# Optimization experiments

Measured on AMD Instinct MI355X. Metric: run time of the kernel, lower is better.

Reference implementation:

```python
import jax, jax.numpy as jnp
import numpy as np

ALPHA, GAMMA, EPS = 0.25, 2.0, 1e-8


def _safe_div(num, den):
    # tf.math.divide_no_nan semantics
    return jnp.where(den > 0, num / jnp.where(den > 0, den, 1.0), 0.0)


def giou_loss(b1, b2):
    """tfa.losses.giou_loss: boxes [ymin, xmin, ymax, xmax], broadcastable
    leading dims; returns 1 - GIoU."""
    b1_ymin, b1_xmin, b1_ymax, b1_xmax = jnp.split(b1, 4, axis=-1)
    b2_ymin, b2_xmin, b2_ymax, b2_xmax = jnp.split(b2, 4, axis=-1)
    b1_area = jnp.maximum(b1_ymax - b1_ymin, 0.0) * jnp.maximum(b1_xmax - b1_xmin, 0.0)
    b2_area = jnp.maximum(b2_ymax - b2_ymin, 0.0) * jnp.maximum(b2_xmax - b2_xmin, 0.0)
    i_ymin = jnp.maximum(b1_ymin, b2_ymin)
    i_xmin = jnp.maximum(b1_xmin, b2_xmin)
    i_ymax = jnp.minimum(b1_ymax, b2_ymax)
    i_xmax = jnp.minimum(b1_xmax, b2_xmax)
    inter = jnp.maximum(i_ymax - i_ymin, 0.0) * jnp.maximum(i_xmax - i_xmin, 0.0)
    union = b1_area + b2_area - inter
    iou = _safe_div(inter, union)
    e_ymin = jnp.minimum(b1_ymin, b2_ymin)
    e_xmin = jnp.minimum(b1_xmin, b2_xmin)
    e_ymax = jnp.maximum(b1_ymax, b2_ymax)
    e_xmax = jnp.maximum(b1_xmax, b2_xmax)
    enclose = jnp.maximum(e_ymax - e_ymin, 0.0) * jnp.maximum(e_xmax - e_xmin, 0.0)
    giou = iou - _safe_div(enclose - union, enclose)
    return (1.0 - giou)[..., 0]  # squeeze the split-kept last dim


def setup_inputs() -> dict:
    key = jax.random.key(0)
    k1, k2, k3, k4 = jax.random.split(key, 4)
    b, n, C, m = 8, 16384, 80, 100
    return {
        "cls_pred": jax.random.uniform(k1, (b, n, C), dtype=jnp.float32),
        "loc_pred": jax.random.uniform(k2, (b, n, 4), dtype=jnp.float32),
        "cls_true": jax.random.randint(k3, (b, m, C), 0, 2, dtype=jnp.int32),
        "loc_true": jax.random.uniform(k4, (b, m, 4), dtype=jnp.float32),
        "reg_mask": jnp.ones((b, m), dtype=jnp.float32),
    }


def reference(cls_pred, loc_pred, cls_true, loc_true, reg_mask):
    b, n, C = cls_pred.shape
    m = cls_true.shape[1]
    ct = (cls_true == 1).astype(jnp.float32)  # (b, m, C)

    # focal-style per-(anchor, class) cost; depends only on cls_pred, so
    # contract against the one-hot target with an einsum instead of
    # materializing a (b, m, n, C) tensor.
    p = cls_pred
    neg_cost = (1.0 - ALPHA) * p ** GAMMA * (-jnp.log(1.0 - p + EPS))
    pos_cost = ALPHA * (1.0 - p) ** GAMMA * (-jnp.log(p + EPS))
    cls_loss = jnp.einsum("bnc,bmc->bmn", pos_cost - neg_cost, ct)  # (b, m, n)

    lt = loc_true[:, :, None, :]  # (b, m, 1, 4)
    lp = loc_pred[:, None, :, :]  # (b, 1, n, 4)
    reg_loss = jnp.sum(jnp.abs(lt - lp), axis=-1)  # (b, m, n)
    giou = giou_loss(lp, lt)  # (b, m, n)

    total = 2.0 * cls_loss + 5.0 * reg_loss + 2.0 * giou
    argmin_total = jnp.argmin(total, axis=-1).astype(jnp.int32)  # (b, m)
    batch = jnp.broadcast_to(jnp.arange(b, dtype=jnp.int32)[:, None], (b, m))
    cls_id = jnp.argmax(ct, axis=-1).astype(jnp.int32)
    return jnp.stack([batch, argmin_total, cls_id], axis=-1)  # (b, m, 3)
```

## Files before the change

### kernel.cpp

```cpp
#include <hip/hip_runtime.h>

constexpr int B = 8, N = 16384, C = 80, M = 100;
constexpr int NT = 64;
constexpr int THREADS = 256;
constexpr int NBLK = N / NT;

typedef _Float16 half8 __attribute__((ext_vector_type(8)));
typedef float f32x4 __attribute__((ext_vector_type(4)));
typedef unsigned long long u64;

constexpr size_t WS_FT   = 0;
constexpr size_t WS_FT2  = 172032;
constexpr size_t WS_CID  = 344064;
constexpr size_t WS_WRED = 347264;

__device__ __forceinline__ unsigned ford(float f) {
    unsigned u = __float_as_uint(f);
    return (u & 0x80000000u) ? ~u : (u | 0x80000000u);
}

__device__ __forceinline__ float rcpf(float x) { return __builtin_amdgcn_rcpf(x); }

__device__ __forceinline__ float pair_total(float cls,
    float4 p, float4 t, float a1, float a2,
    float hp, float wp, float ht, float wt)
{
    float ih = fminf(p.z, t.z) - fmaxf(p.x, t.x);
    float iw = fminf(p.w, t.w) - fmaxf(p.y, t.y);
    float inter = fmaxf(ih, 0.f) * fmaxf(iw, 0.f);
    float uni = a1 + a2 - inter;
    float iou = inter * rcpf(fmaxf(uni, 1e-30f));
    float eh = hp + ht - ih;
    float ew = wp + wt - iw;
    float enc = fmaxf(eh, 0.f) * fmaxf(ew, 0.f);
    float ue = (enc - uni) * rcpf(fmaxf(enc, 1e-30f));
    float rg = fabsf(t.x - p.x) + fabsf(t.y - p.y) +
               fabsf(t.z - p.z) + fabsf(t.w - p.w);
    return fmaf(2.5f, rg, cls) + (ue - iou);
}

__global__ void prep_light(const int* __restrict__ cls_true,
                           uint4* __restrict__ ftab,
                           uint4* __restrict__ ftab2,
                           int* __restrict__ clsid)
{
    int wid = (blockIdx.x * blockDim.x + threadIdx.x) >> 6;
    int l = threadIdx.x & 63;
    if (wid < B * 21) {
        int b = wid / 21, rem = wid % 21, ch = rem / 7, mf = rem % 7;
        int m = mf * 16 + (l & 15);
        int c0 = ch * 32 + (l >> 4) * 8;
        unsigned w[4] = {0, 0, 0, 0};
        if (m < M) {
            const int* row = cls_true + ((size_t)b * M + m) * C;
            #pragma unroll
            for (int e = 0; e < 8; ++e) {
                int c = c0 + e;
                unsigned h = (c < C && row[c] == 1) ? 0x3C00u : 0u;
                w[e >> 1] |= h << ((e & 1) * 16);
            }
        }
        ftab[(size_t)wid * 64 + l] = make_uint4(w[0], w[1], w[2], w[3]);
        ftab2[(size_t)wid * 64 + l] =
            make_uint4(w[0] & 0x10001000u, w[1] & 0x10001000u,
                       w[2] & 0x10001000u, w[3] & 0x10001000u);
    } else if (wid < B * 21 + B * M) {
        int id = wid - B * 21;
        const int* row = cls_true + (size_t)id * C;
        bool v1 = (row[l] == 1);
        bool v2 = (l < 16) ? (row[64 + l] == 1) : false;
        u64 m01 = __ballot(v1);
        u64 m2  = __ballot(v2);
        if (l == 0) {
            int cid = 0;
            if (m01) cid = __ffsll(m01) - 1;
            else if (m2) cid = 64 + __ffsll(m2) - 1;
            clsid[id] = cid;
        }
    }
}

__global__ __launch_bounds__(THREADS, 4)
void match_kernel(const float* __restrict__ cls_pred,
                  const float* __restrict__ loc_pred,
                  const uint4* __restrict__ ftab,
                  const uint4* __restrict__ ftab2,
                  const float* __restrict__ loc_true,
                  u64* __restrict__ wred)
{
    __shared__ u64 s_red[4][112];

    const int b  = blockIdx.y;
    const int n0 = blockIdx.x * NT;
    const int t  = threadIdx.x;
    const int l  = t & 63;
    const int wv = t >> 6;
    const int nw = wv * 16;

    f32x4 acc[7];
    #pragma unroll
    for (int mf = 0; mf < 7; ++mf) acc[mf] = f32x4{0.f, 0.f, 0.f, 0.f};

    const uint4* ft  = ftab  + (size_t)b * 21 * 64;
    const uint4* ft2 = ftab2 + (size_t)b * 21 * 64;
    const float* cpb = cls_pred + (size_t)b * N * 80;
    const int arow = n0 + nw + (l & 15);

    #pragma unroll
    for (int kc = 0; kc < 3; ++kc) {
        const int cbase = kc * 32 + (l >> 4) * 8;
        half8 ah = {0,0,0,0,0,0,0,0}, al = {0,0,0,0,0,0,0,0};
        if (cbase < 80) {
            float4 v0 = *(const float4*)&cpb[(size_t)arow * 80 + cbase];
            float4 v1 = *(const float4*)&cpb[(size_t)arow * 80 + cbase + 4];
            float pv[8] = { v0.x, v0.y, v0.z, v0.w, v1.x, v1.y, v1.z, v1.w };
            #pragma unroll
            for (int j = 0; j < 8; ++j) {
                float p = pv[j], q = 1.0f - p;
                float pos = 0.17328680f * q * q * (-__log2f(p + 1e-8f));
                float neg = 0.51986040f * p * p * (-__log2f(q + 1e-8f));
                float d = pos - neg;
                _Float16 h = (_Float16)d;
                _Float16 r = (_Float16)((d - (float)h) * 2048.0f);
                ah[j] = h;
                al[j] = r;
            }
        }
        #pragma unroll
        for (int mf = 0; mf < 7; ++mf) {
            union { uint4 u; half8 h; } b1, b2;
            b1.u = ft [((size_t)kc * 7 + mf) * 64 + l];
            b2.u = ft2[((size_t)kc * 7 + mf) * 64 + l];
            acc[mf] = __builtin_amdgcn_mfma_f32_16x16x32_f16(ah, b1.h, acc[mf], 0, 0, 0);
            acc[mf] = __builtin_amdgcn_mfma_f32_16x16x32_f16(al, b2.h, acc[mf], 0, 0, 0);
        }
    }

    const int nbase = n0 + nw + (l >> 4) * 4;
    float4 bx[4];
    float a1[4], hp[4], wp[4];
    #pragma unroll
    for (int r = 0; r < 4; ++r) {
        float4 v = ((const float4*)loc_pred)[(size_t)b * N + nbase + r];
        bx[r] = v;
        hp[r] = v.z - v.x;
        wp[r] = v.w - v.y;
        a1[r] = fmaxf(hp[r], 0.f) * fmaxf(wp[r], 0.f);
    }

    #pragma unroll
    for (int mf = 0; mf < 7; ++mf) {
        int m = mf * 16 + (l & 15);
        int mm = (m < M) ? m : (M - 1);
        float4 tb = ((const float4*)loc_true)[(size_t)b * M + mm];
        float ht = tb.z - tb.x, wt = tb.w - tb.y;
        float a2 = fmaxf(ht, 0.f) * fmaxf(wt, 0.f);
        float tot[4];
        #pragma unroll
        for (int r = 0; r < 4; ++r)
            tot[r] = pair_total(acc[mf][r], bx[r], tb, a1[r], a2,
                                hp[r], wp[r], ht, wt);
        float v = tot[0];
        unsigned ni = (unsigned)nbase;
        #pragma unroll
        for (int r = 1; r < 4; ++r) {
            bool c = tot[r] < v;
            v = c ? tot[r] : v;
            ni = c ? (unsigned)(nbase + r) : ni;
        }
        u64 key = ((u64)ford(v) << 32) | ni;
        #pragma unroll
        for (int off = 16; off <= 32; off <<= 1) {
            u64 o = __shfl_xor(key, off, 64);
            key = (o < key) ? o : key;
        }
        if (l < 16) s_red[wv][m] = key;
    }
    __syncthreads();

    if (t < 112) {
        u64 v0 = s_red[0][t], v1 = s_red[1][t];
        u64 v2 = s_red[2][t], v3 = s_red[3][t];
        u64 a = v0 < v1 ? v0 : v1;
        u64 c = v2 < v3 ? v2 : v3;
        a = a < c ? a : c;
        wred[((size_t)b * NBLK + blockIdx.x) * 112 + t] = a;
    }
}

__global__ __launch_bounds__(256)
void reduce_kernel(const u64* __restrict__ wred,
                   const int* __restrict__ clsid,
                   int* __restrict__ out)
{
    __shared__ u64 s_part[4];
    const int bm = blockIdx.x;
    const int b = bm / M, m = bm % M;
    const int t = threadIdx.x, l = t & 63, wv = t >> 6;

    u64 best = wred[((size_t)b * NBLK + t) * 112 + m];
    #pragma unroll
    for (int off = 1; off < 64; off <<= 1) {
        u64 o = __shfl_xor(best, off, 64);
        best = (o < best) ? o : best;
    }
    if (l == 0) s_part[wv] = best;
    __syncthreads();
    if (t == 0) {
        u64 a0 = s_part[0], a1 = s_part[1];
        u64 a2 = s_part[2], a3 = s_part[3];
        u64 a = a0 < a1 ? a0 : a1;
        u64 c = a2 < a3 ? a2 : a3;
        a = a < c ? a : c;
        out[bm * 3 + 0] = b;
        out[bm * 3 + 1] = (int)(unsigned)(a & 0xFFFFFFFFull);
        out[bm * 3 + 2] = clsid[bm];
    }
}

extern "C" void kernel_launch(void* const* d_in, const int* in_sizes, int n_in,
                              void* d_out, int out_size, void* d_ws, size_t ws_size,
                              hipStream_t stream)
{
    const float* cls_pred = (const float*)d_in[0];
    const float* loc_pred = (const float*)d_in[1];
    const int*   cls_true = (const int*)d_in[2];
    const float* loc_true = (const float*)d_in[3];

    char* ws = (char*)d_ws;
    uint4* ftab  = (uint4*)(ws + WS_FT);
    uint4* ftab2 = (uint4*)(ws + WS_FT2);
    int*   clsid = (int*)(ws + WS_CID);
    u64*   wred  = (u64*)(ws + WS_WRED);
    int* out = (int*)d_out;

    int prep_waves = B * 21 + B * M;
    prep_light<<<(prep_waves * 64 + 255) / 256, 256, 0, stream>>>(
        cls_true, ftab, ftab2, clsid);

    dim3 grid(NBLK, B);
    match_kernel<<<grid, THREADS, 0, stream>>>(
        cls_pred, loc_pred, ftab, ftab2, loc_true, wred);

    reduce_kernel<<<B * M, 256, 0, stream>>>(wred, clsid, out);
}
```

Baseline: 46.61 us.

## Double anchor tile per wave to reuse B fragments and shrink reduction

Each wave now handles two 16-anchor M-tiles (NT goes from 64 to 128), so every ftab fragment loaded from global feeds two MFMA chains. The per-lane argmin keys from both tiles are merged before the cross-lane shuffle. Halving the block count halves the partial-result buffer, so the final reduce kernel becomes a single wave that reads two entries per lane with no shared memory. The cost is more accumulator registers (14 f32x4), which may lower occupancy, and half as many blocks for latency hiding.

```diff
diff --git a/kernel.cpp b/kernel.cpp
--- a/kernel.cpp
+++ b/kernel.cpp
@@ -1,7 +1,7 @@
 #include <hip/hip_runtime.h>
 
 constexpr int B = 8, N = 16384, C = 80, M = 100;
-constexpr int NT = 64;
+constexpr int NT = 128;
 constexpr int THREADS = 256;
 constexpr int NBLK = N / NT;
 
@@ -37,6 +37,29 @@
     float rg = fabsf(t.x - p.x) + fabsf(t.y - p.y) +
                fabsf(t.z - p.z) + fabsf(t.w - p.w);
     return fmaf(2.5f, rg, cls) + (ue - iou);
+}
+
+__device__ __forceinline__ void make_frags(const float* __restrict__ cpb,
+                                           int arow, int cbase,
+                                           half8* ah, half8* al)
+{
+    float4 v0 = *(const float4*)&cpb[(size_t)arow * 80 + cbase];
+    float4 v1 = *(const float4*)&cpb[(size_t)arow * 80 + cbase + 4];
+    float pv[8] = { v0.x, v0.y, v0.z, v0.w, v1.x, v1.y, v1.z, v1.w };
+    half8 hh, ll;
+    #pragma unroll
+    for (int j = 0; j < 8; ++j) {
+        float p = pv[j], q = 1.0f - p;
+        float pos = 0.17328680f * q * q * (-__log2f(p + 1e-8f));
+        float neg = 0.51986040f * p * p * (-__log2f(q + 1e-8f));
+        float d = pos - neg;
+        _Float16 h = (_Float16)d;
+        _Float16 r = (_Float16)((d - (float)h) * 2048.0f);
+        hh[j] = h;
+        ll[j] = r;
+    }
+    *ah = hh;
+    *al = ll;
 }
 
 __global__ void prep_light(const int* __restrict__ cls_true,
@@ -95,86 +118,118 @@
     const int t  = threadIdx.x;
     const int l  = t & 63;
     const int wv = t >> 6;
-    const int nw = wv * 16;
-
-    f32x4 acc[7];
-    #pragma unroll
-    for (int mf = 0; mf < 7; ++mf) acc[mf] = f32x4{0.f, 0.f, 0.f, 0.f};
+    const int nw = wv * 32;
+
+    f32x4 acc0[7], acc1[7];
+    #pragma unroll
+    for (int mf = 0; mf < 7; ++mf) {
+        acc0[mf] = f32x4{0.f, 0.f, 0.f, 0.f};
+        acc1[mf] = f32x4{0.f, 0.f, 0.f, 0.f};
+    }
 
     const uint4* ft  = ftab  + (size_t)b * 21 * 64;
     const uint4* ft2 = ftab2 + (size_t)b * 21 * 64;
     const float* cpb = cls_pred + (size_t)b * N * 80;
-    const int arow = n0 + nw + (l & 15);
+    const int arow0 = n0 + nw + (l & 15);
+    const int arow1 = arow0 + 16;
 
     #pragma unroll
     for (int kc = 0; kc < 3; ++kc) {
         const int cbase = kc * 32 + (l >> 4) * 8;
-        half8 ah = {0,0,0,0,0,0,0,0}, al = {0,0,0,0,0,0,0,0};
+        half8 ah0 = {0,0,0,0,0,0,0,0}, al0 = {0,0,0,0,0,0,0,0};
+        half8 ah1 = {0,0,0,0,0,0,0,0}, al1 = {0,0,0,0,0,0,0,0};
         if (cbase < 80) {
-            float4 v0 = *(const float4*)&cpb[(size_t)arow * 80 + cbase];
-            float4 v1 = *(const float4*)&cpb[(size_t)arow * 80 + cbase + 4];
-            float pv[8] = { v0.x, v0.y, v0.z, v0.w, v1.x, v1.y, v1.z, v1.w };
-            #pragma unroll
-            for (int j = 0; j < 8; ++j) {
-                float p = pv[j], q = 1.0f - p;
-                float pos = 0.17328680f * q * q * (-__log2f(p + 1e-8f));
-                float neg = 0.51986040f * p * p * (-__log2f(q + 1e-8f));
-                float d = pos - neg;
-                _Float16 h = (_Float16)d;
-                _Float16 r = (_Float16)((d - (float)h) * 2048.0f);
-                ah[j] = h;
-                al[j] = r;
-            }
+            make_frags(cpb, arow0, cbase, &ah0, &al0);
+            make_frags(cpb, arow1, cbase, &ah1, &al1);
         }
         #pragma unroll
         for (int mf = 0; mf < 7; ++mf) {
             union { uint4 u; half8 h; } b1, b2;
             b1.u = ft [((size_t)kc * 7 + mf) * 64 + l];
             b2.u = ft2[((size_t)kc * 7 + mf) * 64 + l];
-            acc[mf] = __builtin_amdgcn_mfma_f32_16x16x32_f16(ah, b1.h, acc[mf], 0, 0, 0);
-            acc[mf] = __builtin_amdgcn_mfma_f32_16x16x32_f16(al, b2.h, acc[mf], 0, 0, 0);
-        }
-    }
-
-    const int nbase = n0 + nw + (l >> 4) * 4;
-    float4 bx[4];
-    float a1[4], hp[4], wp[4];
-    #pragma unroll
-    for (int r = 0; r < 4; ++r) {
-        float4 v = ((const float4*)loc_pred)[(size_t)b * N + nbase + r];
-        bx[r] = v;
-        hp[r] = v.z - v.x;
-        wp[r] = v.w - v.y;
-        a1[r] = fmaxf(hp[r], 0.f) * fmaxf(wp[r], 0.f);
+            acc0[mf] = __builtin_amdgcn_mfma_f32_16x16x32_f16(ah0, b1.h, acc0[mf], 0, 0, 0);
+            acc0[mf] = __builtin_amdgcn_mfma_f32_16x16x32_f16(al0, b2.h, acc0[mf], 0, 0, 0);
+            acc1[mf] = __builtin_amdgcn_mfma_f32_16x16x32_f16(ah1, b1.h, acc1[mf], 0, 0, 0);
+            acc1[mf] = __builtin_amdgcn_mfma_f32_16x16x32_f16(al1, b2.h, acc1[mf], 0, 0, 0);
+        }
+    }
+
+    u64 key[7];
+
+    {
+        const int nbase = n0 + nw + (l >> 4) * 4;
+        float4 bx[4];
+        float a1[4], hp[4], wp[4];
+        #pragma unroll
+        for (int r = 0; r < 4; ++r) {
+            float4 v = ((const float4*)loc_pred)[(size_t)b * N + nbase + r];
+            bx[r] = v;
+            hp[r] = v.z - v.x;
+            wp[r] = v.w - v.y;
+            a1[r] = fmaxf(hp[r], 0.f) * fmaxf(wp[r], 0.f);
+        }
+        #pragma unroll
+        for (int mf = 0; mf < 7; ++mf) {
+            int m = mf * 16 + (l & 15);
+            int mm = (m < M) ? m : (M - 1);
+            float4 tb = ((const float4*)loc_true)[(size_t)b * M + mm];
+            float ht = tb.z - tb.x, wt = tb.w - tb.y;
+            float a2 = fmaxf(ht, 0.f) * fmaxf(wt, 0.f);
+            float v = pair_total(acc0[mf][0], bx[0], tb, a1[0], a2, hp[0], wp[0], ht, wt);
+            unsigned ni = (unsigned)nbase;
+            #pragma unroll
+            for (int r = 1; r < 4; ++r) {
+                float tr = pair_total(acc0[mf][r], bx[r], tb, a1[r], a2, hp[r], wp[r], ht, wt);
+                bool c = tr < v;
+                v = c ? tr : v;
+                ni = c ? (unsigned)(nbase + r) : ni;
+            }
+            key[mf] = ((u64)ford(v) << 32) | ni;
+        }
+    }
+
+    {
+        const int nbase = n0 + nw + 16 + (l >> 4) * 4;
+        float4 bx[4];
+        float a1[4], hp[4], wp[4];
+        #pragma unroll
+        for (int r = 0; r < 4; ++r) {
+            float4 v = ((const float4*)loc_pred)[(size_t)b * N + nbase + r];
+            bx[r] = v;
+            hp[r] = v.z - v.x;
+            wp[r] = v.w - v.y;
+            a1[r] = fmaxf(hp[r], 0.f) * fmaxf(wp[r], 0.f);
+        }
+        #pragma unroll
+        for (int mf = 0; mf < 7; ++mf) {
+            int m = mf * 16 + (l & 15);
+            int mm = (m < M) ? m : (M - 1);
+            float4 tb = ((const float4*)loc_true)[(size_t)b * M + mm];
+            float ht = tb.z - tb.x, wt = tb.w - tb.y;
+            float a2 = fmaxf(ht, 0.f) * fmaxf(wt, 0.f);
+            float v = pair_total(acc1[mf][0], bx[0], tb, a1[0], a2, hp[0], wp[0], ht, wt);
+            unsigned ni = (unsigned)nbase;
+            #pragma unroll
+            for (int r = 1; r < 4; ++r) {
+                float tr = pair_total(acc1[mf][r], bx[r], tb, a1[r], a2, hp[r], wp[r], ht, wt);
+                bool c = tr < v;
+                v = c ? tr : v;
+                ni = c ? (unsigned)(nbase + r) : ni;
+            }
+            u64 cand = ((u64)ford(v) << 32) | ni;
+            key[mf] = (cand < key[mf]) ? cand : key[mf];
+        }
     }
 
     #pragma unroll
     for (int mf = 0; mf < 7; ++mf) {
-        int m = mf * 16 + (l & 15);
-        int mm = (m < M) ? m : (M - 1);
-        float4 tb = ((const float4*)loc_true)[(size_t)b * M + mm];
-        float ht = tb.z - tb.x, wt = tb.w - tb.y;
-        float a2 = fmaxf(ht, 0.f) * fmaxf(wt, 0.f);
-        float tot[4];
-        #pragma unroll
-        for (int r = 0; r < 4; ++r)
-            tot[r] = pair_total(acc[mf][r], bx[r], tb, a1[r], a2,
-                                hp[r], wp[r], ht, wt);
-        float v = tot[0];
-        unsigned ni = (unsigned)nbase;
-        #pragma unroll
-        for (int r = 1; r < 4; ++r) {
-            bool c = tot[r] < v;
-            v = c ? tot[r] : v;
-            ni = c ? (unsigned)(nbase + r) : ni;
-        }
-        u64 key = ((u64)ford(v) << 32) | ni;
+        u64 k = key[mf];
         #pragma unroll
         for (int off = 16; off <= 32; off <<= 1) {
-            u64 o = __shfl_xor(key, off, 64);
-            key = (o < key) ? o : key;
-        }
-        if (l < 16) s_red[wv][m] = key;
+            u64 o = __shfl_xor(k, off, 64);
+            k = (o < k) ? o : k;
+        }
+        if (l < 16) s_red[wv][mf * 16 + l] = k;
     }
     __syncthreads();
 
@@ -188,32 +243,27 @@
     }
 }
 
-__global__ __launch_bounds__(256)
+__global__ __launch_bounds__(64)
 void reduce_kernel(const u64* __restrict__ wred,
                    const int* __restrict__ clsid,
                    int* __restrict__ out)
 {
-    __shared__ u64 s_part[4];
     const int bm = blockIdx.x;
     const int b = bm / M, m = bm % M;
-    const int t = threadIdx.x, l = t & 63, wv = t >> 6;
-
-    u64 best = wred[((size_t)b * NBLK + t) * 112 + m];
+    const int l = threadIdx.x;
+
+    const u64* base = wred + (size_t)b * NBLK * 112 + m;
+    u64 k0 = base[(size_t)l * 112];
+    u64 k1 = base[(size_t)(l + 64) * 112];
+    u64 best = (k0 < k1) ? k0 : k1;
     #pragma unroll
     for (int off = 1; off < 64; off <<= 1) {
         u64 o = __shfl_xor(best, off, 64);
         best = (o < best) ? o : best;
     }
-    if (l == 0) s_part[wv] = best;
-    __syncthreads();
-    if (t == 0) {
-        u64 a0 = s_part[0], a1 = s_part[1];
-        u64 a2 = s_part[2], a3 = s_part[3];
-        u64 a = a0 < a1 ? a0 : a1;
-        u64 c = a2 < a3 ? a2 : a3;
-        a = a < c ? a : c;
+    if (l == 0) {
         out[bm * 3 + 0] = b;
-        out[bm * 3 + 1] = (int)(unsigned)(a & 0xFFFFFFFFull);
+        out[bm * 3 + 1] = (int)(unsigned)(best & 0xFFFFFFFFull);
         out[bm * 3 + 2] = clsid[bm];
     }
 }
@@ -242,5 +292,5 @@
     match_kernel<<<grid, THREADS, 0, stream>>>(
         cls_pred, loc_pred, ftab, ftab2, loc_true, wred);
 
-    reduce_kernel<<<B * M, 256, 0, stream>>>(wred, clsid, out);
-}
+    reduce_kernel<<<B * M, 64, 0, stream>>>(wred, clsid, out);
+}
```

New measurement: 94.24 us. +102.2%, slower.

## Stage one-hot B fragments in LDS and derive the low-half fragment in registers

Applied to the files above, without the earlier changes.

Drops the second one-hot table (ftab2) and derives its masked fragment in registers from the first table with a bitwise AND. Each block copies its batch's fragment table (21.5 KB) into shared memory after a barrier, so the per-fragment B loads come from LDS instead of global memory or L2. The cls_pred loads are hoisted ahead of the staging copy so their latency overlaps it. This costs 21.5 KB of LDS per block, which may limit occupancy, plus an extra barrier, and every block now copies the whole table even though it only reads each entry once.

```diff
diff --git a/kernel.cpp b/kernel.cpp
--- a/kernel.cpp
+++ b/kernel.cpp
@@ -4,15 +4,15 @@
 constexpr int NT = 64;
 constexpr int THREADS = 256;
 constexpr int NBLK = N / NT;
+constexpr int NFRAG = 21 * 64;
 
 typedef _Float16 half8 __attribute__((ext_vector_type(8)));
 typedef float f32x4 __attribute__((ext_vector_type(4)));
 typedef unsigned long long u64;
 
 constexpr size_t WS_FT   = 0;
-constexpr size_t WS_FT2  = 172032;
-constexpr size_t WS_CID  = 344064;
-constexpr size_t WS_WRED = 347264;
+constexpr size_t WS_CID  = 172032;
+constexpr size_t WS_WRED = 175232;
 
 __device__ __forceinline__ unsigned ford(float f) {
     unsigned u = __float_as_uint(f);
@@ -39,9 +39,28 @@
     return fmaf(2.5f, rg, cls) + (ue - iou);
 }
 
+__device__ __forceinline__ void make_frags(float4 v0, float4 v1,
+                                           half8* ah, half8* al)
+{
+    float pv[8] = { v0.x, v0.y, v0.z, v0.w, v1.x, v1.y, v1.z, v1.w };
+    half8 hh, ll;
+    #pragma unroll
+    for (int j = 0; j < 8; ++j) {
+        float p = pv[j], q = 1.0f - p;
+        float pos = 0.17328680f * q * q * (-__log2f(p + 1e-8f));
+        float neg = 0.51986040f * p * p * (-__log2f(q + 1e-8f));
+        float d = pos - neg;
+        _Float16 h = (_Float16)d;
+        _Float16 r = (_Float16)((d - (float)h) * 2048.0f);
+        hh[j] = h;
+        ll[j] = r;
+    }
+    *ah = hh;
+    *al = ll;
+}
+
 __global__ void prep_light(const int* __restrict__ cls_true,
                            uint4* __restrict__ ftab,
-                           uint4* __restrict__ ftab2,
                            int* __restrict__ clsid)
 {
     int wid = (blockIdx.x * blockDim.x + threadIdx.x) >> 6;
@@ -61,9 +80,6 @@
             }
         }
         ftab[(size_t)wid * 64 + l] = make_uint4(w[0], w[1], w[2], w[3]);
-        ftab2[(size_t)wid * 64 + l] =
-            make_uint4(w[0] & 0x10001000u, w[1] & 0x10001000u,
-                       w[2] & 0x10001000u, w[3] & 0x10001000u);
     } else if (wid < B * 21 + B * M) {
         int id = wid - B * 21;
         const int* row = cls_true + (size_t)id * C;
@@ -84,10 +100,10 @@
 void match_kernel(const float* __restrict__ cls_pred,
                   const float* __restrict__ loc_pred,
                   const uint4* __restrict__ ftab,
-                  const uint4* __restrict__ ftab2,
                   const float* __restrict__ loc_true,
                   u64* __restrict__ wred)
 {
+    __shared__ uint4 s_ft[NFRAG];
     __shared__ u64 s_red[4][112];
 
     const int b  = blockIdx.y;
@@ -97,40 +113,38 @@
     const int wv = t >> 6;
     const int nw = wv * 16;
 
-    f32x4 acc[7];
-    #pragma unroll
-    for (int mf = 0; mf < 7; ++mf) acc[mf] = f32x4{0.f, 0.f, 0.f, 0.f};
-
-    const uint4* ft  = ftab  + (size_t)b * 21 * 64;
-    const uint4* ft2 = ftab2 + (size_t)b * 21 * 64;
     const float* cpb = cls_pred + (size_t)b * N * 80;
     const int arow = n0 + nw + (l & 15);
+
+    float4 av0[3], av1[3];
+    #pragma unroll
+    for (int kc = 0; kc < 3; ++kc) {
+        const int cbase = kc * 32 + (l >> 4) * 8;
+        if (cbase < 80) {
+            av0[kc] = *(const float4*)&cpb[(size_t)arow * 80 + cbase];
+            av1[kc] = *(const float4*)&cpb[(size_t)arow * 80 + cbase + 4];
+        }
+    }
+
+    const uint4* ftb = ftab + (size_t)b * NFRAG;
+    for (int i = t; i < NFRAG; i += THREADS) s_ft[i] = ftb[i];
+    __syncthreads();
+
+    f32x4 acc[7];
+    #pragma unroll
+    for (int mf = 0; mf < 7; ++mf) acc[mf] = f32x4{0.f, 0.f, 0.f, 0.f};
 
     #pragma unroll
     for (int kc = 0; kc < 3; ++kc) {
         const int cbase = kc * 32 + (l >> 4) * 8;
         half8 ah = {0,0,0,0,0,0,0,0}, al = {0,0,0,0,0,0,0,0};
-        if (cbase < 80) {
-            float4 v0 = *(const float4*)&cpb[(size_t)arow * 80 + cbase];
-            float4 v1 = *(const float4*)&cpb[(size_t)arow * 80 + cbase + 4];
-            float pv[8] = { v0.x, v0.y, v0.z, v0.w, v1.x, v1.y, v1.z, v1.w };
-            #pragma unroll
-            for (int j = 0; j < 8; ++j) {
-                float p = pv[j], q = 1.0f - p;
-                float pos = 0.17328680f * q * q * (-__log2f(p + 1e-8f));
-                float neg = 0.51986040f * p * p * (-__log2f(q + 1e-8f));
-                float d = pos - neg;
-                _Float16 h = (_Float16)d;
-                _Float16 r = (_Float16)((d - (float)h) * 2048.0f);
-                ah[j] = h;
-                al[j] = r;
-            }
-        }
+        if (cbase < 80) make_frags(av0[kc], av1[kc], &ah, &al);
         #pragma unroll
         for (int mf = 0; mf < 7; ++mf) {
             union { uint4 u; half8 h; } b1, b2;
-            b1.u = ft [((size_t)kc * 7 + mf) * 64 + l];
-            b2.u = ft2[((size_t)kc * 7 + mf) * 64 + l];
+            b1.u = s_ft[(kc * 7 + mf) * 64 + l];
+            b2.u = make_uint4(b1.u.x & 0x10001000u, b1.u.y & 0x10001000u,
+                              b1.u.z & 0x10001000u, b1.u.w & 0x10001000u);
             acc[mf] = __builtin_amdgcn_mfma_f32_16x16x32_f16(ah, b1.h, acc[mf], 0, 0, 0);
             acc[mf] = __builtin_amdgcn_mfma_f32_16x16x32_f16(al, b2.h, acc[mf], 0, 0, 0);
         }
@@ -229,18 +243,17 @@
 
     char* ws = (char*)d_ws;
     uint4* ftab  = (uint4*)(ws + WS_FT);
-    uint4* ftab2 = (uint4*)(ws + WS_FT2);
     int*   clsid = (int*)(ws + WS_CID);
     u64*   wred  = (u64*)(ws + WS_WRED);
     int* out = (int*)d_out;
 
     int prep_waves = B * 21 + B * M;
     prep_light<<<(prep_waves * 64 + 255) / 256, 256, 0, stream>>>(
-        cls_true, ftab, ftab2, clsid);
+        cls_true, ftab, clsid);
 
     dim3 grid(NBLK, B);
     match_kernel<<<grid, THREADS, 0, stream>>>(
-        cls_pred, loc_pred, ftab, ftab2, loc_true, wred);
+        cls_pred, loc_pred, ftab, loc_true, wred);
 
     reduce_kernel<<<B * M, 256, 0, stream>>>(wred, clsid, out);
 }
```

Measured after the change: 45.68 us. -2.0%, faster.
